# Kernel tuning notes

Measured on AMD Instinct MI355X. Metric: run time of the kernel, lower is better.

## Reference

```python
import jax, jax.numpy as jnp
import numpy as np

B, S, LC, DIM, H, FFN = 1, 3600, 512, 1536, 12, 8960
HD = DIM // H          # 128
GRID = (4, 30, 30)     # f*h*w == S
K_LEN = 9900           # hardcoded k_lens in SelfAttention.forward
EPS = 1e-6

def _rope_axis_angles(n_pos, dim):
    inv = 1.0 / np.power(10000.0, np.arange(0, dim, 2, dtype=np.float64) / dim)
    return np.outer(np.arange(n_pos), inv)

def _build_rope(grid, head_dim):
    c = head_dim // 2                      # 64
    c1, c2 = c - 2 * (c // 3), c // 3      # 22, 21 (Wan 3D rope split)
    f, h, w = grid
    af = _rope_axis_angles(f, 2 * c1)
    ah = _rope_axis_angles(h, 2 * c2)
    aw = _rope_axis_angles(w, 2 * c2)
    ang = np.concatenate([
        np.broadcast_to(af[:, None, None, :], (f, h, w, c1)),
        np.broadcast_to(ah[None, :, None, :], (f, h, w, c2)),
        np.broadcast_to(aw[None, None, :, :], (f, h, w, c2)),
    ], axis=-1).reshape(f * h * w, c)
    return np.cos(ang).astype(np.float32), np.sin(ang).astype(np.float32)

def setup_inputs():
    key = jax.random.key(0)
    ks = iter(jax.random.split(key, 40))
    cos, sin = _build_rope(GRID, HD)
    inp = {
        'x': jax.random.normal(next(ks), (B, S, DIM), dtype=jnp.float32),
        'context': jax.random.normal(next(ks), (B, LC, DIM), dtype=jnp.float32),
        't_mod': 0.1 * jax.random.normal(next(ks), (B, 6, DIM), dtype=jnp.float32),
        'rope_cos': jnp.asarray(cos), 'rope_sin': jnp.asarray(sin),
        'modulation': jax.random.normal(next(ks), (1, 6, DIM), dtype=jnp.float32) / DIM ** 0.5,
    }
    for p in ('sa', 'ca'):
        for w in ('q', 'k', 'v', 'o'):
            inp[p + '_' + w + 'w'] = 0.02 * jax.random.normal(next(ks), (DIM, DIM), dtype=jnp.float32)
            inp[p + '_' + w + 'b'] = jnp.zeros((DIM,), jnp.float32)
        inp[p + '_nq'] = jnp.ones((DIM,), jnp.float32)
        inp[p + '_nk'] = jnp.ones((DIM,), jnp.float32)
    inp['n3_w'] = jnp.ones((DIM,), jnp.float32)
    inp['n3_b'] = jnp.zeros((DIM,), jnp.float32)
    inp['ffn_w1'] = 0.02 * jax.random.normal(next(ks), (DIM, FFN), dtype=jnp.float32)
    inp['ffn_b1'] = jnp.zeros((FFN,), jnp.float32)
    inp['ffn_w2'] = 0.02 * jax.random.normal(next(ks), (FFN, DIM), dtype=jnp.float32)
    inp['ffn_b2'] = jnp.zeros((DIM,), jnp.float32)
    return inp

def _rms(x, w):
    x32 = x.astype(jnp.float32)
    n = x32 * jax.lax.rsqrt(jnp.mean(x32 * x32, axis=-1, keepdims=True) + EPS)
    return n.astype(x.dtype) * w

def _ln(x, w=None, b=None):
    mu = jnp.mean(x, axis=-1, keepdims=True)
    var = jnp.mean(jnp.square(x - mu), axis=-1, keepdims=True)
    y = (x - mu) * jax.lax.rsqrt(var + EPS)
    return y if w is None else y * w + b

def _rope(x, cos, sin):
    b, s, h, d = x.shape
    x2 = x.reshape(b, s, h, d // 2, 2)
    xe, xo = x2[..., 0], x2[..., 1]
    c, sn = cos[None, :, None, :], sin[None, :, None, :]
    return jnp.stack([xe * c - xo * sn, xe * sn + xo * c], axis=-1).reshape(b, s, h, d)

def _attn(q, k, v, k_len=None):
    # q,k,v: [B,S,H,D]
    scores = jnp.einsum('bqhd,bkhd->bhqk', q, k) * (q.shape[-1] ** -0.5)
    if k_len is not None:
        mask = jnp.arange(k.shape[1]) < k_len
        scores = jnp.where(mask[None, None, None, :], scores, jnp.finfo(scores.dtype).min)
    return jnp.einsum('bhqk,bkhd->bqhd', jax.nn.softmax(scores, axis=-1), v)

def reference(x, context, t_mod, rope_cos, rope_sin, modulation,
              sa_qw, sa_qb, sa_kw, sa_kb, sa_vw, sa_vb, sa_ow, sa_ob, sa_nq, sa_nk,
              ca_qw, ca_qb, ca_kw, ca_kb, ca_vw, ca_vb, ca_ow, ca_ob, ca_nq, ca_nk,
              n3_w, n3_b, ffn_w1, ffn_b1, ffn_w2, ffn_b2):
    mod = modulation + t_mod                      # [B,6,DIM]
    sh_msa, sc_msa, g_msa, sh_mlp, sc_mlp, g_mlp = [mod[:, i:i + 1] for i in range(6)]
    b = x.shape[0]
    # --- self-attention with AdaLN modulate + 3D RoPE + k_lens mask ---
    h = _ln(x) * (1 + sc_msa) + sh_msa
    q = _rms(h @ sa_qw + sa_qb, sa_nq).reshape(b, -1, H, HD)
    k = _rms(h @ sa_kw + sa_kb, sa_nk).reshape(b, -1, H, HD)
    v = (h @ sa_vw + sa_vb).reshape(b, -1, H, HD)
    a = _attn(_rope(q, rope_cos, rope_sin), _rope(k, rope_cos, rope_sin), v, k_len=K_LEN)
    x = x + g_msa * (a.reshape(b, -1, DIM) @ sa_ow + sa_ob)
    # --- cross-attention ---
    hc = _ln(x, n3_w, n3_b)
    q = _rms(hc @ ca_qw + ca_qb, ca_nq).reshape(b, -1, H, HD)
    k = _rms(context @ ca_kw + ca_kb, ca_nk).reshape(b, -1, H, HD)
    v = (context @ ca_vw + ca_vb).reshape(b, -1, H, HD)
    x = x + (_attn(q, k, v).reshape(b, -1, DIM) @ ca_ow + ca_ob)
    # --- gated FFN with AdaLN modulate ---
    h = _ln(x) * (1 + sc_mlp) + sh_mlp
    h = jax.nn.gelu(h @ ffn_w1 + ffn_b1, approximate=True) @ ffn_w2 + ffn_b2
    return x + g_mlp * h
```

## Files before the change

kernel.cpp:

```cpp
#include <hip/hip_runtime.h>
#include <cstdint>

#define S_LEN 3600
#define DMODEL 1536
#define LCTX 512
#define NH 12
#define HDIM 128
#define FFND 8960
#define SPAD_SELF 3648

typedef short v8s __attribute__((ext_vector_type(8)));
typedef float v4f __attribute__((ext_vector_type(4)));
typedef unsigned short u16b;
typedef unsigned int u32b;

#define AS1 __attribute__((address_space(1)))
#define AS3 __attribute__((address_space(3)))

__device__ __forceinline__ void gl_lds16(const void* g, void* l){
  __builtin_amdgcn_global_load_lds((AS1 const void*)g, (AS3 void*)l, 16, 0, 0);
}

__device__ __forceinline__ u16b f2b(float f){
  union { float f; u32b i; } x; x.f = f;
// ... 68 lines not shown
  int hd = tid >> 1, kc = (tid & 1) * 16;
  u16b* dst = Vt + ((size_t)h * HDIM + hd) * Spad + kb + kc;
  #pragma unroll
  for (int e = 0; e < 16; e += 2){
    u32b pk = ((u32b)t[kc + e][hd]) | (((u32b)t[kc + e + 1][hd]) << 16);
    *(u32b*)(dst + e) = pk;
  }
}

__global__ __launch_bounds__(256) void ln_mod(const float* __restrict__ X,
                                              const float* __restrict__ gamma,
                                              const float* __restrict__ beta,
                                              float gadd, u16b* __restrict__ out){
  int row = blockIdx.x;
  const float* xr = X + (size_t)row * DMODEL;
  int tid = threadIdx.x;
  float v[6]; float s1 = 0.f, s2 = 0.f;
  #pragma unroll
  for (int j = 0; j < 6; ++j){ v[j] = xr[tid + j * 256]; s1 += v[j]; s2 += v[j] * v[j]; }
  #pragma unroll
  for (int o = 1; o < 64; o <<= 1){ s1 += __shfl_xor(s1, o); s2 += __shfl_xor(s2, o); }
  __shared__ float red[8];
  int wid = tid >> 6, lane = tid & 63;
  if (!lane){ red[wid * 2] = s1; red[wid * 2 + 1] = s2; }
  __syncthreads();
  s1 = red[0] + red[2] + red[4] + red[6];
  s2 = red[1] + red[3] + red[5] + red[7];
  float mu = s1 / DMODEL;
  float var = s2 / DMODEL - mu * mu;
  float rstd = rsqrtf(var + 1e-6f);
  #pragma unroll
  for (int j = 0; j < 6; ++j){
    int c = tid + j * 256;
    float g = gamma[c] + gadd;
    float b = beta[c];
    out[(size_t)row * DMODEL + c] = f2b((v[j] - mu) * rstd * g + b);
  }
}

__global__ __launch_bounds__(256) void rms_rope(const float* __restrict__ X,
                                                const float* __restrict__ w,
                                                const float* __restrict__ cosT,
                                                const float* __restrict__ sinT,
                                                float qmul,
                                                u16b* __restrict__ out){
  int row = blockIdx.x;
  const float* xr = X + (size_t)row * DMODEL;
  int tid = threadIdx.x;
  float2 v[3]; float ss = 0.f;
  #pragma unroll
  for (int j = 0; j < 3; ++j){
    v[j] = *(const float2*)(xr + 2 * (tid + j * 256));
    ss += v[j].x * v[j].x + v[j].y * v[j].y;
  }
  #pragma unroll
  for (int o = 1; o < 64; o <<= 1) ss += __shfl_xor(ss, o);
  __shared__ float red[4];
  int wid = tid >> 6, lane = tid & 63;
  if (!lane) red[wid] = ss;
  __syncthreads();
  ss = red[0] + red[1] + red[2] + red[3];
  float rstd = rsqrtf(ss / DMODEL + 1e-6f);
  #pragma unroll
  for (int j = 0; j < 3; ++j){
    int p = tid + j * 256;
    float xe = v[j].x * rstd * w[2 * p];
    float xo = v[j].y * rstd * w[2 * p + 1];
    float oe, oo;
    if (cosT){
      int d = p & 63;
      float c = cosT[row * 64 + d], sn = sinT[row * 64 + d];
      oe = xe * c - xo * sn; oo = xe * sn + xo * c;
    } else { oe = xe; oo = xo; }
    oe *= qmul; oo *= qmul;
    u32b packed = ((u32b)f2b(oe)) | (((u32b)f2b(oo)) << 16);
    *(u32b*)(out + (size_t)row * DMODEL + 2 * p) = packed;
  }
}

struct Seg { const float* bias; float* outF; u16b* outB; };
struct Segs { Seg s[3]; };

template<int EPI>
__global__ __launch_bounds__(256, 2) void gemm_bt(
    const u16b* __restrict__ A, const u16b* __restrict__ BT,
    const float* __restrict__ bias, const float* __restrict__ res,
    const float* __restrict__ gate, float* __restrict__ outF,
    u16b* __restrict__ outB, int M, int N, int K, int kLen)
{
  __shared__ char Ls[3][16384];
  const int tid = threadIdx.x, lane = tid & 63, wid = tid >> 6;
  const int nwg = gridDim.x * gridDim.y;
  const int swz = xcd_swz(blockIdx.x + gridDim.x * blockIdx.y, nwg);
  const int bm = (swz % gridDim.x) * 128, bn = (swz / gridDim.x) * 128;
  const int kbase = blockIdx.z * kLen;
  const int wm = (wid >> 1) * 64, wn = (wid & 1) * 64;
  v4f acc[4][4] = {};

  auto stage = [&](int buf, int t){
    int k0 = kbase + t * 32;
    #pragma unroll
    for (int c = 0; c < 2; ++c){
      int seg = wid * 2 + c;
      int l = seg * 64 + lane;
      int row = l >> 2, cs = l & 3;
      int col = cs ^ swz4(row);
      gl_lds16(A + (size_t)min(bm + row, M - 1) * K + k0 + col * 8,
               Ls[buf] + seg * 1024);
      gl_lds16(BT + (size_t)(bn + row) * K + k0 + col * 8,
               Ls[buf] + 8192 + seg * 1024);
    }
  };

  const int nt = kLen / 32;
  stage(0, 0);
  stage(1, 1);
  const int chk = lane >> 4, qr = lane & 15;
  for (int t = 0; t < nt; ++t){
    if (t + 1 < nt) asm volatile("s_waitcnt vmcnt(4)" ::: "memory");
    else            asm volatile("s_waitcnt vmcnt(0)" ::: "memory");
    __builtin_amdgcn_s_barrier();
    if (t + 2 < nt) stage((t + 2) % 3, t + 2);
    char* Ab = Ls[t % 3]; char* Bb = Ab + 8192;
    v8s af[4], bfr[4];
    #pragma unroll
    for (int f = 0; f < 4; ++f){
      int rowa = wm + f * 16 + qr;
      af[f] = *(const v8s*)(Ab + rowa * 64 + ((chk ^ swz4(rowa)) * 16));
      int rowb = wn + f * 16 + qr;
      bfr[f] = *(const v8s*)(Bb + rowb * 64 + ((chk ^ swz4(rowb)) * 16));
    }
    __builtin_amdgcn_s_setprio(1);
    #pragma unroll
    for (int i = 0; i < 4; ++i)
      #pragma unroll
      for (int j = 0; j < 4; ++j)
        acc[i][j] = __builtin_amdgcn_mfma_f32_16x16x32_bf16(af[i], bfr[j], acc[i][j], 0, 0, 0);
    __builtin_amdgcn_s_setprio(0);
  }
  const int rr = lane >> 4;
  #pragma unroll
  for (int i = 0; i < 4; ++i){
    #pragma unroll
    for (int j = 0; j < 4; ++j){
      int n = bn + wn + j * 16 + qr;
      float bv = (EPI != 5 && bias) ? bias[n] : 0.f;
      float gv = (EPI == 2 && gate) ? gate[n] : 1.f;
      #pragma unroll
      for (int r = 0; r < 4; ++r){
        int m = bm + wm + i * 16 + rr * 4 + r;
        if (m < M){
          float val = acc[i][j][r] + bv;
          size_t idx = (size_t)m * N + n;
          if (EPI == 1) outF[idx] = val;
          else if (EPI == 2) outF[idx] = res[idx] + gv * val;
          else if (EPI == 5) outF[(size_t)blockIdx.z * M * N + idx] = val;
          else {
            float t3 = val * val * val;
            float g = val / (1.f + __expf(-1.5957691216057308f * (val + 0.044715f * t3)));
            outB[idx] = f2b(g);
          }
        }
      }
    }
  }
}

__global__ __launch_bounds__(256, 2) void gemm_seg(
    const u16b* __restrict__ A, const u16b* __restrict__ BT,
    Segs segs, int M, int N, int K)
{
  __shared__ char Ls[3][16384];
  const int tid = threadIdx.x, lane = tid & 63, wid = tid >> 6;
  const int nwg = gridDim.x * gridDim.y;
  const int swz = xcd_swz(blockIdx.x + gridDim.x * blockIdx.y, nwg);
  const int bm = (swz % gridDim.x) * 128, bn = (swz / gridDim.x) * 128;
  const int wm = (wid >> 1) * 64, wn = (wid & 1) * 64;
  v4f acc[4][4] = {};

  auto stage = [&](int buf, int t){
    int k0 = t * 32;
    #pragma unroll
    for (int c = 0; c < 2; ++c){
      int seg = wid * 2 + c;
      int l = seg * 64 + lane;
      int row = l >> 2, cs = l & 3;
      int col = cs ^ swz4(row);
      gl_lds16(A + (size_t)min(bm + row, M - 1) * K + k0 + col * 8,
               Ls[buf] + seg * 1024);
      gl_lds16(BT + (size_t)(bn + row) * K + k0 + col * 8,
               Ls[buf] + 8192 + seg * 1024);
    }
  };

  const int nt = K / 32;
  stage(0, 0);
  stage(1, 1);
  const int chk = lane >> 4, qr = lane & 15;
  for (int t = 0; t < nt; ++t){
    if (t + 1 < nt) asm volatile("s_waitcnt vmcnt(4)" ::: "memory");
    else            asm volatile("s_waitcnt vmcnt(0)" ::: "memory");
    __builtin_amdgcn_s_barrier();
    if (t + 2 < nt) stage((t + 2) % 3, t + 2);
    char* Ab = Ls[t % 3]; char* Bb = Ab + 8192;
    v8s af[4], bfr[4];
    #pragma unroll
    for (int f = 0; f < 4; ++f){
      int rowa = wm + f * 16 + qr;
      af[f] = *(const v8s*)(Ab + rowa * 64 + ((chk ^ swz4(rowa)) * 16));
      int rowb = wn + f * 16 + qr;
      bfr[f] = *(const v8s*)(Bb + rowb * 64 + ((chk ^ swz4(rowb)) * 16));
    }
    __builtin_amdgcn_s_setprio(1);
    #pragma unroll
    for (int i = 0; i < 4; ++i)
      #pragma unroll
      for (int j = 0; j < 4; ++j)
        acc[i][j] = __builtin_amdgcn_mfma_f32_16x16x32_bf16(af[i], bfr[j], acc[i][j], 0, 0, 0);
    __builtin_amdgcn_s_setprio(0);
  }
  const int seg = bn / 1536;
  const Seg sg = segs.s[seg];
  const int rr = lane >> 4;
  #pragma unroll
  for (int i = 0; i < 4; ++i){
    #pragma unroll
    for (int j = 0; j < 4; ++j){
      int nloc = bn - seg * 1536 + wn + j * 16 + qr;
      float bv = sg.bias[nloc];
      #pragma unroll
      for (int r = 0; r < 4; ++r){
        int m = bm + wm + i * 16 + rr * 4 + r;
        if (m < M){
          float val = acc[i][j][r] + bv;
          size_t idx = (size_t)m * 1536 + nloc;
          if (sg.outB) sg.outB[idx] = f2b(val);
          else sg.outF[idx] = val;
        }
      }
    }
  }
}

__global__ __launch_bounds__(256) void ffn2_reduce(const float* __restrict__ part,
                                                   const float* __restrict__ res,
                                                   const float* __restrict__ bias,
                                                   const float* __restrict__ gate,
                                                   float* __restrict__ out, int total){
  int i4 = blockIdx.x * 256 + threadIdx.x;
  if (i4 * 4 >= total) return;
  int base = i4 * 4;
  int n = base % DMODEL;
  float4 p0 = *(const float4*)(part + base);
  float4 p1 = *(const float4*)(part + (size_t)total + base);
  float4 p2 = *(const float4*)(part + 2 * (size_t)total + base);
  float4 p3 = *(const float4*)(part + 3 * (size_t)total + base);
  float4 rs = *(const float4*)(res + base);
  float4 bv = *(const float4*)(bias + n);
  float4 gv = *(const float4*)(gate + n);
  float4 o;
  o.x = rs.x + gv.x * (p0.x + p1.x + p2.x + p3.x + bv.x);
  o.y = rs.y + gv.y * (p0.y + p1.y + p2.y + p3.y + bv.y);
  o.z = rs.z + gv.z * (p0.z + p1.z + p2.z + p3.z + bv.z);
  o.w = rs.w + gv.w * (p0.w + p1.w + p2.w + p3.w + bv.w);
  *(float4*)(out + base) = o;
}

__global__ __launch_bounds__(256) void merge_o(const float* __restrict__ op0,
                                               const float* __restrict__ op1,
                                               const float2* __restrict__ ml,
                                               u16b* __restrict__ outO, int Sq){
  int i4 = blockIdx.x * 256 + threadIdx.x;
  const int perRow = DMODEL / 4;
  if (i4 >= Sq * perRow) return;
  int row = i4 / perRow, c4 = (i4 % perRow) * 4;
  int h = c4 >> 7;
  float2 ml0 = ml[h * Sq + row];
  float2 ml1 = ml[NH * Sq + h * Sq + row];
  float M = fmaxf(ml0.x, ml1.x);
  float w0 = exp2f(ml0.x - M), w1 = exp2f(ml1.x - M);
  float inv = 1.f / (ml0.y * w0 + ml1.y * w1);
  float4 a = *(const float4*)(op0 + (size_t)row * DMODEL + c4);
  float4 b = *(const float4*)(op1 + (size_t)row * DMODEL + c4);
  u32b lo = ((u32b)f2b((a.x * w0 + b.x * w1) * inv)) | (((u32b)f2b((a.y * w0 + b.y * w1) * inv)) << 16);
  u32b hi = ((u32b)f2b((a.z * w0 + b.z * w1) * inv)) | (((u32b)f2b((a.w * w0 + b.w * w1) * inv)) << 16);
  uint2 w2; w2.x = lo; w2.y = hi;
  *(uint2*)(outO + (size_t)row * DMODEL + c4) = w2;
}

__global__ __launch_bounds__(256, 4) void flash_attn(
    const u16b* __restrict__ Q, const u16b* __restrict__ Kp,
    const u16b* __restrict__ Vt, u16b* __restrict__ O,
    float* __restrict__ op0, float* __restrict__ op1,
    float2* __restrict__ mlbuf,
    int Sq, int Sk, int ksplit, int Spad)
{
  __shared__ char KV[32768];
  __shared__ char Pall[8192];
  const int tid = threadIdx.x, lane = tid & 63, wid = tid >> 6;
  const int h = blockIdx.y;
  const int z = blockIdx.z;
  const int kbeg = z * ksplit;
  const int kend = min(kbeg + ksplit, Sk);
  const int q0 = blockIdx.x * 64 + wid * 16;
  const int qq = lane & 15, cc = lane >> 4;
  char* Kb = KV; char* Vb = KV + 16384;
  char* Pb = Pall + wid * 2048;

  v8s qf[4];
  {
    int qrow = min(q0 + qq, Sq - 1);
    const u16b* qp = Q + (size_t)qrow * DMODEL + h * HDIM + cc * 8;
    #pragma unroll
    for (int ks = 0; ks < 4; ++ks) qf[ks] = *(const v8s*)(qp + ks * 32);
  }

  auto stage = [&](int kb0){
    #pragma unroll
    for (int c = 0; c < 4; ++c){
      int seg = wid * 4 + c;
      int g = seg * 64 + lane;
      int krow = g >> 4, kcol = (g & 15) ^ (krow & 7);
      gl_lds16(Kp + (size_t)min(kb0 + krow, Sk - 1) * DMODEL + h * HDIM + kcol * 8,
               Kb + seg * 1024);
// ... 116 lines not shown
        if (qrow < Sq)
          O[(size_t)qrow * DMODEL + h * HDIM + hdb * 16 + qq] = f2b(oacc[hdb][r] * lr[r]);
      }
  }
}

extern "C" void kernel_launch(void* const* d_in, const int* in_sizes, int n_in,
                              void* d_out, int out_size, void* d_ws, size_t ws_size,
                              hipStream_t stream){
  (void)in_sizes; (void)n_in; (void)out_size; (void)ws_size;
  const float* x     = (const float*)d_in[0];
  const float* ctx   = (const float*)d_in[1];
  const float* t_mod = (const float*)d_in[2];
  const float* ropec = (const float*)d_in[3];
  const float* ropes = (const float*)d_in[4];
  const float* modu  = (const float*)d_in[5];
  const float* sa_qw = (const float*)d_in[6];  const float* sa_qb = (const float*)d_in[7];
  const float* sa_kw = (const float*)d_in[8];  const float* sa_kb = (const float*)d_in[9];
  const float* sa_vw = (const float*)d_in[10]; const float* sa_vb = (const float*)d_in[11];
  const float* sa_ow = (const float*)d_in[12]; const float* sa_ob = (const float*)d_in[13];
  const float* sa_nq = (const float*)d_in[14]; const float* sa_nk = (const float*)d_in[15];
  const float* ca_qw = (const float*)d_in[16]; const float* ca_qb = (const float*)d_in[17];
  const float* ca_kw = (const float*)d_in[18]; const float* ca_kb = (const float*)d_in[19];
  const float* ca_vw = (const float*)d_in[20]; const float* ca_vb = (const float*)d_in[21];
  const float* ca_ow = (const float*)d_in[22]; const float* ca_ob = (const float*)d_in[23];
  const float* ca_nq = (const float*)d_in[24]; const float* ca_nk = (const float*)d_in[25];
  const float* n3w   = (const float*)d_in[26]; const float* n3b   = (const float*)d_in[27];
  const float* fw1   = (const float*)d_in[28]; const float* fb1   = (const float*)d_in[29];
  const float* fw2   = (const float*)d_in[30]; const float* fb2   = (const float*)d_in[31];
  float* out = (float*)d_out;

  const float QSCALE = 0.08838834764831845f * 1.4426950408889634f;

  char* wsp = (char*)d_ws;
  size_t off = 0;
  auto alloc = [&](size_t b){ void* p = wsp + off; off += (b + 255) & ~(size_t)255; return p; };
  const size_t WW = (size_t)DMODEL * DMODEL * 2;
  float* modc = (float*)alloc(6 * DMODEL * 4);
  u16b* w1T   = (u16b*)alloc((size_t)FFND * DMODEL * 2);
  u16b* w2T   = (u16b*)alloc((size_t)DMODEL * FFND * 2);
  u16b* h_bf  = (u16b*)alloc((size_t)S_LEN * DMODEL * 2);
  float* pre0 = (float*)alloc((size_t)S_LEN * DMODEL * 4);
  size_t region0 = off;
  u16b* sa_qkvT = (u16b*)alloc(3 * WW);
  u16b* sa_owT  = (u16b*)alloc(WW);
  u16b* ca_qwT  = (u16b*)alloc(WW);
  u16b* ca_kvT  = (u16b*)alloc(2 * WW);
  u16b* ca_owT  = (u16b*)alloc(WW);
  float* x2    = (float*)alloc((size_t)S_LEN * DMODEL * 4);
  float* pre2  = (float*)alloc((size_t)LCTX * DMODEL * 4);
  u16b* qb     = (u16b*)alloc((size_t)S_LEN * DMODEL * 2);
  u16b* kb     = (u16b*)alloc((size_t)S_LEN * DMODEL * 2);
  u16b* vb     = (u16b*)alloc((size_t)S_LEN * DMODEL * 2);
  u16b* ab     = (u16b*)alloc((size_t)S_LEN * DMODEL * 2);
  u16b* ctxb   = (u16b*)alloc((size_t)LCTX * DMODEL * 2);
  u16b* k2b    = (u16b*)alloc((size_t)LCTX * DMODEL * 2);
  u16b* v2b    = (u16b*)alloc((size_t)LCTX * DMODEL * 2);
  u16b* vts    = (u16b*)alloc((size_t)NH * HDIM * SPAD_SELF * 2);
  u16b* vtc    = (u16b*)alloc((size_t)NH * HDIM * LCTX * 2);
  u16b* fmid = (u16b*)(wsp + region0);
  float* fpart = (float*)(wsp + region0 + (size_t)S_LEN * FFND * 2);

  add_vec<<<36, 256, 0, stream>>>(modu, t_mod, modc, 6 * DMODEL);

  WJobs jobs; int t = 0;
  auto addjob = [&](int i, const float* w_, u16b* wt, int K, int N){
    jobs.j[i].W = w_; jobs.j[i].WT = wt; jobs.j[i].K = K; jobs.j[i].N = N; jobs.j[i].t0 = t;
    t += (K / 32) * (N / 32);
  };
  addjob(0, sa_qw, sa_qkvT, DMODEL, DMODEL);
  addjob(1, sa_kw, sa_qkvT + (size_t)DMODEL * DMODEL, DMODEL, DMODEL);
  addjob(2, sa_vw, sa_qkvT + (size_t)2 * DMODEL * DMODEL, DMODEL, DMODEL);
  addjob(3, sa_ow, sa_owT, DMODEL, DMODEL);
  addjob(4, ca_qw, ca_qwT, DMODEL, DMODEL);
  addjob(5, ca_kw, ca_kvT, DMODEL, DMODEL);
  addjob(6, ca_vw, ca_kvT + (size_t)DMODEL * DMODEL, DMODEL, DMODEL);
  addjob(7, ca_ow, ca_owT, DMODEL, DMODEL);
  addjob(8, fw1, w1T, DMODEL, FFND);
  addjob(9, fw2, w2T, FFND, DMODEL);
  wconv<<<t, 256, 0, stream>>>(jobs);

  f2b_kernel<<<(LCTX * DMODEL) / 256, 256, 0, stream>>>(ctx, ctxb, LCTX * DMODEL);

  ln_mod<<<S_LEN, 256, 0, stream>>>(x, modc + DMODEL, modc, 1.f, h_bf);
  dim3 g12(29, 12);
  {
    Segs sg;
    sg.s[0] = { sa_qb, pre0, nullptr };
    sg.s[1] = { sa_kb, x2,   nullptr };
    sg.s[2] = { sa_vb, nullptr, vb   };
    gemm_seg<<<dim3(29, 36), 256, 0, stream>>>(h_bf, sa_qkvT, sg, S_LEN, 3 * DMODEL, DMODEL);
  }
  rms_rope<<<S_LEN, 256, 0, stream>>>(pre0, sa_nq, ropec, ropes, QSCALE, qb);
  rms_rope<<<S_LEN, 256, 0, stream>>>(x2, sa_nk, ropec, ropes, 1.f, kb);
  vtrans<<<dim3(SPAD_SELF / 32, 12), 256, 0, stream>>>(vb, vts, S_LEN, SPAD_SELF);
  flash_attn<<<dim3(57, 12, 2), 256, 0, stream>>>(qb, kb, vts, ab,
      (float*)pre0, (float*)x2, (float2*)vb, S_LEN, S_LEN, 1856, SPAD_SELF);
  merge_o<<<(S_LEN * (DMODEL / 4) + 255) / 256, 256, 0, stream>>>(
      (const float*)pre0, (const float*)x2, (const float2*)vb, ab, S_LEN);
  gemm_bt<2><<<g12, 256, 0, stream>>>(ab, sa_owT, sa_ob, x, modc + 2 * DMODEL, x2, nullptr, S_LEN, DMODEL, DMODEL, DMODEL);

  ln_mod<<<S_LEN, 256, 0, stream>>>(x2, n3w, n3b, 0.f, h_bf);
  gemm_bt<1><<<g12, 256, 0, stream>>>(h_bf, ca_qwT, ca_qb, nullptr, nullptr, pre0, nullptr, S_LEN, DMODEL, DMODEL, DMODEL);
  {
    Segs sg;
    sg.s[0] = { ca_kb, pre2, nullptr };
    sg.s[1] = { ca_vb, nullptr, v2b  };
    sg.s[2] = { ca_vb, nullptr, v2b  };
    gemm_seg<<<dim3(4, 24), 256, 0, stream>>>(ctxb, ca_kvT, sg, LCTX, 2 * DMODEL, DMODEL);
  }
  rms_rope<<<S_LEN, 256, 0, stream>>>(pre0, ca_nq, nullptr, nullptr, QSCALE, qb);
  rms_rope<<<LCTX, 256, 0, stream>>>(pre2, ca_nk, nullptr, nullptr, 1.f, k2b);
  vtrans<<<dim3(16, 12), 256, 0, stream>>>(v2b, vtc, LCTX, LCTX);
  flash_attn<<<dim3(57, 12, 2), 256, 0, stream>>>(qb, k2b, vtc, ab,
      (float*)pre0, (float*)kb, (float2*)vts, S_LEN, LCTX, 256, LCTX);
  merge_o<<<(S_LEN * (DMODEL / 4) + 255) / 256, 256, 0, stream>>>(
      (const float*)pre0, (const float*)kb, (const float2*)vts, ab, S_LEN);
  gemm_bt<2><<<g12, 256, 0, stream>>>(ab, ca_owT, ca_ob, x2, nullptr, pre0, nullptr, S_LEN, DMODEL, DMODEL, DMODEL);

  ln_mod<<<S_LEN, 256, 0, stream>>>(pre0, modc + 4 * DMODEL, modc + 3 * DMODEL, 1.f, h_bf);
  gemm_bt<3><<<dim3(29, 70), 256, 0, stream>>>(h_bf, w1T, fb1, nullptr, nullptr, nullptr, fmid, S_LEN, FFND, DMODEL, DMODEL);
  gemm_bt<5><<<dim3(29, 12, 4), 256, 0, stream>>>(fmid, w2T, nullptr, nullptr, nullptr, fpart, nullptr, S_LEN, DMODEL, FFND, FFND / 4);
  ffn2_reduce<<<(S_LEN * DMODEL / 4 + 255) / 256, 256, 0, stream>>>(fpart, pre0, fb2, modc + 5 * DMODEL, out, S_LEN * DMODEL);
}
```

Baseline: 964.5 us.

## Add 128x256-tile GEMM for QKV and FFN, precompute load pointers and offsets

Adds a gemm_w kernel with 128x256 output tiles (each wave computes 64x128) and a 1D XCD-swizzled grid. It is used for the fused QKV projection, FFN up-projection with GELU, and the split-K FFN down-projection. The wider tile raises arithmetic intensity and reuse of the A tile in LDS, at the cost of more accumulator registers (32 v4f per wave) and 72KB of LDS per block, which may limit occupancy. The existing GEMMs also switch to precomputed, incrementing global pointers and precomputed LDS fragment offsets to cut address arithmetic in the inner loop.

```diff
diff --git a/kernel.cpp b/kernel.cpp
--- a/kernel.cpp
+++ b/kernel.cpp
@@ -174,6 +174,124 @@
 struct Segs { Seg s[3]; };
 
 template<int EPI>
+__global__ __launch_bounds__(256, 2) void gemm_w(
+    const u16b* __restrict__ A, const u16b* __restrict__ BT,
+    Segs segs, const float* __restrict__ bias,
+    float* __restrict__ outF, u16b* __restrict__ outB,
+    int M, int N, int K, int kLen, int nxM)
+{
+  __shared__ char Lsf[3 * 24576];
+  const int tid = threadIdx.x, lane = tid & 63, wid = tid >> 6;
+  const int swz = xcd_swz(blockIdx.x, gridDim.x);
+  const int bx = swz % nxM;
+  const int byz = swz / nxM;
+  const int nyN = N / 256;
+  const int by = (EPI == 2) ? (byz % nyN) : byz;
+  const int z  = (EPI == 2) ? (byz / nyN) : 0;
+  const int bm = bx * 128, bn = by * 256;
+  const int kbase = z * kLen;
+  const int wm = (wid >> 1) * 64, wn = (wid & 1) * 128;
+  const int qr = lane & 15, chk = lane >> 4;
+  v4f acc[4][8] = {};
+
+  const u16b* pA[2]; const u16b* pB[4];
+  #pragma unroll
+  for (int c = 0; c < 2; ++c){
+    int row = c * 64 + (tid >> 2);
+    int col = (tid & 3) ^ swz4(row);
+    pA[c] = A + (size_t)min(bm + row, M - 1) * K + kbase + col * 8;
+  }
+  #pragma unroll
+  for (int c = 0; c < 4; ++c){
+    int row = c * 64 + (tid >> 2);
+    int col = (tid & 3) ^ swz4(row);
+    pB[c] = BT + (size_t)(bn + row) * K + kbase + col * 8;
+  }
+  auto stage = [&](int b){
+    char* Lb = Lsf + b * 24576;
+    #pragma unroll
+    for (int c = 0; c < 2; ++c){
+      gl_lds16(pA[c], Lb + (c * 256 + tid) * 16);
+      pA[c] += 32;
+    }
+    #pragma unroll
+    for (int c = 0; c < 4; ++c){
+      gl_lds16(pB[c], Lb + 8192 + (c * 256 + tid) * 16);
+      pB[c] += 32;
+    }
+  };
+
+  int offA[4], offB[8];
+  #pragma unroll
+  for (int fr = 0; fr < 4; ++fr){
+    int r = wm + fr * 16 + qr;
+    offA[fr] = r * 64 + ((chk ^ swz4(r)) * 16);
+  }
+  #pragma unroll
+  for (int fc = 0; fc < 8; ++fc){
+    int r = wn + fc * 16 + qr;
+    offB[fc] = 8192 + r * 64 + ((chk ^ swz4(r)) * 16);
+  }
+
+  const int nt = kLen / 32;
+  stage(0); stage(1);
+  int s = 0, sp = 2;
+  for (int t = 0; t < nt; ++t){
+    if (t + 1 < nt) asm volatile("s_waitcnt vmcnt(6)" ::: "memory");
+    else            asm volatile("s_waitcnt vmcnt(0)" ::: "memory");
+    __builtin_amdgcn_s_barrier();
+    if (t + 2 < nt) stage(sp);
+    char* Lb = Lsf + s * 24576;
+    v8s af[4], bf[8];
+    #pragma unroll
+    for (int fr = 0; fr < 4; ++fr) af[fr] = *(const v8s*)(Lb + offA[fr]);
+    #pragma unroll
+    for (int fc = 0; fc < 8; ++fc) bf[fc] = *(const v8s*)(Lb + offB[fc]);
+    __builtin_amdgcn_s_setprio(1);
+    #pragma unroll
+    for (int fr = 0; fr < 4; ++fr)
+      #pragma unroll
+      for (int fc = 0; fc < 8; ++fc)
+        acc[fr][fc] = __builtin_amdgcn_mfma_f32_16x16x32_bf16(af[fr], bf[fc], acc[fr][fc], 0, 0, 0);
+    __builtin_amdgcn_s_setprio(0);
+    s = (s == 2) ? 0 : s + 1;
+    sp = (sp == 2) ? 0 : sp + 1;
+  }
+
+  const int rr = lane >> 4;
+  #pragma unroll
+  for (int fr = 0; fr < 4; ++fr){
+    #pragma unroll
+    for (int fc = 0; fc < 8; ++fc){
+      int n = bn + wn + fc * 16 + qr;
+      #pragma unroll
+      for (int r = 0; r < 4; ++r){
+        int m = bm + wm + fr * 16 + rr * 4 + r;
+        if (m < M){
+          float val = acc[fr][fc][r];
+          if (EPI == 0){
+            int sgi = n / 1536;
+            Seg sg = segs.s[sgi];
+            int nloc = n - sgi * 1536;
+            float v2 = val + sg.bias[nloc];
+            size_t idx = (size_t)m * 1536 + nloc;
+            if (sg.outB) sg.outB[idx] = f2b(v2);
+            else sg.outF[idx] = v2;
+          } else if (EPI == 1){
+            float v2 = val + bias[n];
+            float t3 = v2 * v2 * v2;
+            float g = v2 / (1.f + __expf(-1.5957691216057308f * (v2 + 0.044715f * t3)));
+            outB[(size_t)m * N + n] = f2b(g);
+          } else {
+            outF[(size_t)z * M * 1536 + (size_t)m * 1536 + n] = val;
+          }
+        }
+      }
+    }
+  }
+}
+
+template<int EPI>
 __global__ __launch_bounds__(256, 2) void gemm_bt(
     const u16b* __restrict__ A, const u16b* __restrict__ BT,
     const float* __restrict__ bias, const float* __restrict__ res,
@@ -189,38 +307,48 @@
   const int wm = (wid >> 1) * 64, wn = (wid & 1) * 64;
   v4f acc[4][4] = {};
 
-  auto stage = [&](int buf, int t){
-    int k0 = kbase + t * 32;
+  const u16b* pA[2]; const u16b* pB[2];
+  #pragma unroll
+  for (int c = 0; c < 2; ++c){
+    int row = c * 64 + (tid >> 2);
+    int col = (tid & 3) ^ swz4(row);
+    pA[c] = A + (size_t)min(bm + row, M - 1) * K + kbase + col * 8;
+    pB[c] = BT + (size_t)(bn + row) * K + kbase + col * 8;
+  }
+  auto stage = [&](int b){
+    char* Lb = Ls[b];
     #pragma unroll
     for (int c = 0; c < 2; ++c){
-      int seg = wid * 2 + c;
-      int l = seg * 64 + lane;
-      int row = l >> 2, cs = l & 3;
-      int col = cs ^ swz4(row);
-      gl_lds16(A + (size_t)min(bm + row, M - 1) * K + k0 + col * 8,
-               Ls[buf] + seg * 1024);
-      gl_lds16(BT + (size_t)(bn + row) * K + k0 + col * 8,
-               Ls[buf] + 8192 + seg * 1024);
+      gl_lds16(pA[c], Lb + (c * 256 + tid) * 16);
+      gl_lds16(pB[c], Lb + 8192 + (c * 256 + tid) * 16);
+      pA[c] += 32; pB[c] += 32;
     }
   };
 
+  const int chk = lane >> 4, qr = lane & 15;
+  int offA[4], offB[4];
+  #pragma unroll
+  for (int f = 0; f < 4; ++f){
+    int ra = wm + f * 16 + qr;
+    offA[f] = ra * 64 + ((chk ^ swz4(ra)) * 16);
+    int rb = wn + f * 16 + qr;
+    offB[f] = 8192 + rb * 64 + ((chk ^ swz4(rb)) * 16);
+  }
+
   const int nt = kLen / 32;
-  stage(0, 0);
-  stage(1, 1);
-  const int chk = lane >> 4, qr = lane & 15;
+  stage(0); stage(1);
+  int s = 0, sp = 2;
   for (int t = 0; t < nt; ++t){
     if (t + 1 < nt) asm volatile("s_waitcnt vmcnt(4)" ::: "memory");
     else            asm volatile("s_waitcnt vmcnt(0)" ::: "memory");
     __builtin_amdgcn_s_barrier();
-    if (t + 2 < nt) stage((t + 2) % 3, t + 2);
-    char* Ab = Ls[t % 3]; char* Bb = Ab + 8192;
+    if (t + 2 < nt) stage(sp);
+    char* Lb = Ls[s];
     v8s af[4], bfr[4];
     #pragma unroll
     for (int f = 0; f < 4; ++f){
-      int rowa = wm + f * 16 + qr;
-      af[f] = *(const v8s*)(Ab + rowa * 64 + ((chk ^ swz4(rowa)) * 16));
-      int rowb = wn + f * 16 + qr;
-      bfr[f] = *(const v8s*)(Bb + rowb * 64 + ((chk ^ swz4(rowb)) * 16));
+      af[f] = *(const v8s*)(Lb + offA[f]);
+      bfr[f] = *(const v8s*)(Lb + offB[f]);
     }
     __builtin_amdgcn_s_setprio(1);
     #pragma unroll
@@ -229,6 +357,8 @@
       for (int j = 0; j < 4; ++j)
         acc[i][j] = __builtin_amdgcn_mfma_f32_16x16x32_bf16(af[i], bfr[j], acc[i][j], 0, 0, 0);
     __builtin_amdgcn_s_setprio(0);
+    s = (s == 2) ? 0 : s + 1;
+    sp = (sp == 2) ? 0 : sp + 1;
   }
   const int rr = lane >> 4;
   #pragma unroll
@@ -236,7 +366,7 @@
     #pragma unroll
     for (int j = 0; j < 4; ++j){
       int n = bn + wn + j * 16 + qr;
-      float bv = (EPI != 5 && bias) ? bias[n] : 0.f;
+      float bv = bias ? bias[n] : 0.f;
       float gv = (EPI == 2 && gate) ? gate[n] : 1.f;
       #pragma unroll
       for (int r = 0; r < 4; ++r){
@@ -245,13 +375,7 @@
           float val = acc[i][j][r] + bv;
           size_t idx = (size_t)m * N + n;
           if (EPI == 1) outF[idx] = val;
-          else if (EPI == 2) outF[idx] = res[idx] + gv * val;
-          else if (EPI == 5) outF[(size_t)blockIdx.z * M * N + idx] = val;
-          else {
-            float t3 = val * val * val;
-            float g = val / (1.f + __expf(-1.5957691216057308f * (val + 0.044715f * t3)));
-            outB[idx] = f2b(g);
-          }
+          else outF[idx] = res[idx] + gv * val;
         }
       }
     }
@@ -270,38 +394,48 @@
   const int wm = (wid >> 1) * 64, wn = (wid & 1) * 64;
   v4f acc[4][4] = {};
 
-  auto stage = [&](int buf, int t){
-    int k0 = t * 32;
+  const u16b* pA[2]; const u16b* pB[2];
+  #pragma unroll
+  for (int c = 0; c < 2; ++c){
+    int row = c * 64 + (tid >> 2);
+    int col = (tid & 3) ^ swz4(row);
+    pA[c] = A + (size_t)min(bm + row, M - 1) * K + col * 8;
+    pB[c] = BT + (size_t)(bn + row) * K + col * 8;
+  }
+  auto stage = [&](int b){
+    char* Lb = Ls[b];
     #pragma unroll
     for (int c = 0; c < 2; ++c){
-      int seg = wid * 2 + c;
-      int l = seg * 64 + lane;
-      int row = l >> 2, cs = l & 3;
-      int col = cs ^ swz4(row);
-      gl_lds16(A + (size_t)min(bm + row, M - 1) * K + k0 + col * 8,
-               Ls[buf] + seg * 1024);
-      gl_lds16(BT + (size_t)(bn + row) * K + k0 + col * 8,
-               Ls[buf] + 8192 + seg * 1024);
+      gl_lds16(pA[c], Lb + (c * 256 + tid) * 16);
+      gl_lds16(pB[c], Lb + 8192 + (c * 256 + tid) * 16);
+      pA[c] += 32; pB[c] += 32;
     }
   };
 
+  const int chk = lane >> 4, qr = lane & 15;
+  int offA[4], offB[4];
+  #pragma unroll
+  for (int f = 0; f < 4; ++f){
+    int ra = wm + f * 16 + qr;
+    offA[f] = ra * 64 + ((chk ^ swz4(ra)) * 16);
+    int rb = wn + f * 16 + qr;
+    offB[f] = 8192 + rb * 64 + ((chk ^ swz4(rb)) * 16);
+  }
+
   const int nt = K / 32;
-  stage(0, 0);
-  stage(1, 1);
-  const int chk = lane >> 4, qr = lane & 15;
+  stage(0); stage(1);
+  int s = 0, sp = 2;
   for (int t = 0; t < nt; ++t){
     if (t + 1 < nt) asm volatile("s_waitcnt vmcnt(4)" ::: "memory");
     else            asm volatile("s_waitcnt vmcnt(0)" ::: "memory");
     __builtin_amdgcn_s_barrier();
-    if (t + 2 < nt) stage((t + 2) % 3, t + 2);
-    char* Ab = Ls[t % 3]; char* Bb = Ab + 8192;
+    if (t + 2 < nt) stage(sp);
+    char* Lb = Ls[s];
     v8s af[4], bfr[4];
     #pragma unroll
     for (int f = 0; f < 4; ++f){
-      int rowa = wm + f * 16 + qr;
-      af[f] = *(const v8s*)(Ab + rowa * 64 + ((chk ^ swz4(rowa)) * 16));
-      int rowb = wn + f * 16 + qr;
-      bfr[f] = *(const v8s*)(Bb + rowb * 64 + ((chk ^ swz4(rowb)) * 16));
+      af[f] = *(const v8s*)(Lb + offA[f]);
+      bfr[f] = *(const v8s*)(Lb + offB[f]);
     }
     __builtin_amdgcn_s_setprio(1);
     #pragma unroll
@@ -310,6 +444,8 @@
       for (int j = 0; j < 4; ++j)
         acc[i][j] = __builtin_amdgcn_mfma_f32_16x16x32_bf16(af[i], bfr[j], acc[i][j], 0, 0, 0);
     __builtin_amdgcn_s_setprio(0);
+    s = (s == 2) ? 0 : s + 1;
+    sp = (sp == 2) ? 0 : sp + 1;
   }
   const int seg = bn / 1536;
   const Seg sg = segs.s[seg];
@@ -614,6 +750,8 @@
 
   f2b_kernel<<<(LCTX * DMODEL) / 256, 256, 0, stream>>>(ctx, ctxb, LCTX * DMODEL);
 
+  Segs dummy = {};
+
   ln_mod<<<S_LEN, 256, 0, stream>>>(x, modc + DMODEL, modc, 1.f, h_bf);
   dim3 g12(29, 12);
   {
@@ -621,7 +759,8 @@
     sg.s[0] = { sa_qb, pre0, nullptr };
     sg.s[1] = { sa_kb, x2,   nullptr };
     sg.s[2] = { sa_vb, nullptr, vb   };
-    gemm_seg<<<dim3(29, 36), 256, 0, stream>>>(h_bf, sa_qkvT, sg, S_LEN, 3 * DMODEL, DMODEL);
+    gemm_w<0><<<29 * 18, 256, 0, stream>>>(h_bf, sa_qkvT, sg, nullptr, nullptr, nullptr,
+                                           S_LEN, 3 * DMODEL, DMODEL, DMODEL, 29);
   }
   rms_rope<<<S_LEN, 256, 0, stream>>>(pre0, sa_nq, ropec, ropes, QSCALE, qb);
   rms_rope<<<S_LEN, 256, 0, stream>>>(x2, sa_nk, ropec, ropes, 1.f, kb);
@@ -651,7 +790,9 @@
   gemm_bt<2><<<g12, 256, 0, stream>>>(ab, ca_owT, ca_ob, x2, nullptr, pre0, nullptr, S_LEN, DMODEL, DMODEL, DMODEL);
 
   ln_mod<<<S_LEN, 256, 0, stream>>>(pre0, modc + 4 * DMODEL, modc + 3 * DMODEL, 1.f, h_bf);
-  gemm_bt<3><<<dim3(29, 70), 256, 0, stream>>>(h_bf, w1T, fb1, nullptr, nullptr, nullptr, fmid, S_LEN, FFND, DMODEL, DMODEL);
-  gemm_bt<5><<<dim3(29, 12, 4), 256, 0, stream>>>(fmid, w2T, nullptr, nullptr, nullptr, fpart, nullptr, S_LEN, DMODEL, FFND, FFND / 4);
+  gemm_w<1><<<29 * 35, 256, 0, stream>>>(h_bf, w1T, dummy, fb1, nullptr, fmid,
+                                         S_LEN, FFND, DMODEL, DMODEL, 29);
+  gemm_w<2><<<29 * 6 * 4, 256, 0, stream>>>(fmid, w2T, dummy, nullptr, fpart, nullptr,
+                                            S_LEN, DMODEL, FFND, FFND / 4, 29);
   ffn2_reduce<<<(S_LEN * DMODEL / 4 + 255) / 256, 256, 0, stream>>>(fpart, pre0, fb2, modc + 5 * DMODEL, out, S_LEN * DMODEL);
 }
```

Result: slower. 1.036 ms (+7.4%).

## Split-K the 1536x1536 GEMMs into two halves and add a reduce kernel

Applied to the files above, without the earlier changes.

The three square DMODEL GEMMs (self-attn output, cross-attn Q, cross-attn output) now run split-K with two K-halves. This doubles the grid from 348 to 696 workgroups to fill more CUs. Each half writes fp32 partials into reused scratch buffers, and a new red2 kernel sums them and applies bias, gate and residual. The GEMM main loops also precompute global and LDS pointers/offsets instead of recomputing indices each iteration. The trade is extra partial-sum memory traffic and an added kernel launch per GEMM, plus reliance on aliasing scratch buffers (including the sa_qkvT weights buffer) that must be dead at that point.

```diff
diff --git a/kernel.cpp b/kernel.cpp
--- a/kernel.cpp
+++ b/kernel.cpp
@@ -176,9 +176,9 @@
 template<int EPI>
 __global__ __launch_bounds__(256, 2) void gemm_bt(
     const u16b* __restrict__ A, const u16b* __restrict__ BT,
-    const float* __restrict__ bias, const float* __restrict__ res,
-    const float* __restrict__ gate, float* __restrict__ outF,
-    u16b* __restrict__ outB, int M, int N, int K, int kLen)
+    const float* __restrict__ bias, float* __restrict__ outF,
+    float* __restrict__ outF2, u16b* __restrict__ outB,
+    int M, int N, int K, int kLen)
 {
   __shared__ char Ls[3][16384];
   const int tid = threadIdx.x, lane = tid & 63, wid = tid >> 6;
@@ -189,38 +189,48 @@
   const int wm = (wid >> 1) * 64, wn = (wid & 1) * 64;
   v4f acc[4][4] = {};
 
-  auto stage = [&](int buf, int t){
-    int k0 = kbase + t * 32;
+  const u16b* pA[2]; const u16b* pB[2];
+  #pragma unroll
+  for (int c = 0; c < 2; ++c){
+    int row = c * 64 + (tid >> 2);
+    int col = (tid & 3) ^ swz4(row);
+    pA[c] = A + (size_t)min(bm + row, M - 1) * K + kbase + col * 8;
+    pB[c] = BT + (size_t)(bn + row) * K + kbase + col * 8;
+  }
+  auto stage = [&](int b){
+    char* Lb = Ls[b];
     #pragma unroll
     for (int c = 0; c < 2; ++c){
-      int seg = wid * 2 + c;
-      int l = seg * 64 + lane;
-      int row = l >> 2, cs = l & 3;
-      int col = cs ^ swz4(row);
-      gl_lds16(A + (size_t)min(bm + row, M - 1) * K + k0 + col * 8,
-               Ls[buf] + seg * 1024);
-      gl_lds16(BT + (size_t)(bn + row) * K + k0 + col * 8,
-               Ls[buf] + 8192 + seg * 1024);
+      gl_lds16(pA[c], Lb + (c * 256 + tid) * 16);
+      gl_lds16(pB[c], Lb + 8192 + (c * 256 + tid) * 16);
+      pA[c] += 32; pB[c] += 32;
     }
   };
 
+  const int chk = lane >> 4, qr = lane & 15;
+  int offA[4], offB[4];
+  #pragma unroll
+  for (int f = 0; f < 4; ++f){
+    int ra = wm + f * 16 + qr;
+    offA[f] = ra * 64 + ((chk ^ swz4(ra)) * 16);
+    int rb = wn + f * 16 + qr;
+    offB[f] = 8192 + rb * 64 + ((chk ^ swz4(rb)) * 16);
+  }
+
   const int nt = kLen / 32;
-  stage(0, 0);
-  stage(1, 1);
-  const int chk = lane >> 4, qr = lane & 15;
+  stage(0); stage(1);
+  int s = 0, sp = 2;
   for (int t = 0; t < nt; ++t){
     if (t + 1 < nt) asm volatile("s_waitcnt vmcnt(4)" ::: "memory");
     else            asm volatile("s_waitcnt vmcnt(0)" ::: "memory");
     __builtin_amdgcn_s_barrier();
-    if (t + 2 < nt) stage((t + 2) % 3, t + 2);
-    char* Ab = Ls[t % 3]; char* Bb = Ab + 8192;
+    if (t + 2 < nt) stage(sp);
+    char* Lb = Ls[s];
     v8s af[4], bfr[4];
     #pragma unroll
     for (int f = 0; f < 4; ++f){
-      int rowa = wm + f * 16 + qr;
-      af[f] = *(const v8s*)(Ab + rowa * 64 + ((chk ^ swz4(rowa)) * 16));
-      int rowb = wn + f * 16 + qr;
-      bfr[f] = *(const v8s*)(Bb + rowb * 64 + ((chk ^ swz4(rowb)) * 16));
+      af[f] = *(const v8s*)(Lb + offA[f]);
+      bfr[f] = *(const v8s*)(Lb + offB[f]);
     }
     __builtin_amdgcn_s_setprio(1);
     #pragma unroll
@@ -229,28 +239,31 @@
       for (int j = 0; j < 4; ++j)
         acc[i][j] = __builtin_amdgcn_mfma_f32_16x16x32_bf16(af[i], bfr[j], acc[i][j], 0, 0, 0);
     __builtin_amdgcn_s_setprio(0);
+    s = (s == 2) ? 0 : s + 1;
+    sp = (sp == 2) ? 0 : sp + 1;
   }
   const int rr = lane >> 4;
+  float* op6 = (EPI == 6) ? (blockIdx.z ? outF2 : outF) : outF;
   #pragma unroll
   for (int i = 0; i < 4; ++i){
     #pragma unroll
     for (int j = 0; j < 4; ++j){
       int n = bn + wn + j * 16 + qr;
-      float bv = (EPI != 5 && bias) ? bias[n] : 0.f;
-      float gv = (EPI == 2 && gate) ? gate[n] : 1.f;
+      float bv = (EPI == 3) ? bias[n] : 0.f;
       #pragma unroll
       for (int r = 0; r < 4; ++r){
         int m = bm + wm + i * 16 + rr * 4 + r;
         if (m < M){
           float val = acc[i][j][r] + bv;
           size_t idx = (size_t)m * N + n;
-          if (EPI == 1) outF[idx] = val;
-          else if (EPI == 2) outF[idx] = res[idx] + gv * val;
-          else if (EPI == 5) outF[(size_t)blockIdx.z * M * N + idx] = val;
-          else {
+          if (EPI == 3){
             float t3 = val * val * val;
             float g = val / (1.f + __expf(-1.5957691216057308f * (val + 0.044715f * t3)));
             outB[idx] = f2b(g);
+          } else if (EPI == 5){
+            outF[(size_t)blockIdx.z * M * N + idx] = val;
+          } else {
+            op6[idx] = val;
           }
         }
       }
@@ -270,38 +283,48 @@
   const int wm = (wid >> 1) * 64, wn = (wid & 1) * 64;
   v4f acc[4][4] = {};
 
-  auto stage = [&](int buf, int t){
-    int k0 = t * 32;
+  const u16b* pA[2]; const u16b* pB[2];
+  #pragma unroll
+  for (int c = 0; c < 2; ++c){
+    int row = c * 64 + (tid >> 2);
+    int col = (tid & 3) ^ swz4(row);
+    pA[c] = A + (size_t)min(bm + row, M - 1) * K + col * 8;
+    pB[c] = BT + (size_t)(bn + row) * K + col * 8;
+  }
+  auto stage = [&](int b){
+    char* Lb = Ls[b];
     #pragma unroll
     for (int c = 0; c < 2; ++c){
-      int seg = wid * 2 + c;
-      int l = seg * 64 + lane;
-      int row = l >> 2, cs = l & 3;
-      int col = cs ^ swz4(row);
-      gl_lds16(A + (size_t)min(bm + row, M - 1) * K + k0 + col * 8,
-               Ls[buf] + seg * 1024);
-      gl_lds16(BT + (size_t)(bn + row) * K + k0 + col * 8,
-               Ls[buf] + 8192 + seg * 1024);
+      gl_lds16(pA[c], Lb + (c * 256 + tid) * 16);
+      gl_lds16(pB[c], Lb + 8192 + (c * 256 + tid) * 16);
+      pA[c] += 32; pB[c] += 32;
     }
   };
 
+  const int chk = lane >> 4, qr = lane & 15;
+  int offA[4], offB[4];
+  #pragma unroll
+  for (int f = 0; f < 4; ++f){
+    int ra = wm + f * 16 + qr;
+    offA[f] = ra * 64 + ((chk ^ swz4(ra)) * 16);
+    int rb = wn + f * 16 + qr;
+    offB[f] = 8192 + rb * 64 + ((chk ^ swz4(rb)) * 16);
+  }
+
   const int nt = K / 32;
-  stage(0, 0);
-  stage(1, 1);
-  const int chk = lane >> 4, qr = lane & 15;
+  stage(0); stage(1);
+  int s = 0, sp = 2;
   for (int t = 0; t < nt; ++t){
     if (t + 1 < nt) asm volatile("s_waitcnt vmcnt(4)" ::: "memory");
     else            asm volatile("s_waitcnt vmcnt(0)" ::: "memory");
     __builtin_amdgcn_s_barrier();
-    if (t + 2 < nt) stage((t + 2) % 3, t + 2);
-    char* Ab = Ls[t % 3]; char* Bb = Ab + 8192;
+    if (t + 2 < nt) stage(sp);
+    char* Lb = Ls[s];
     v8s af[4], bfr[4];
     #pragma unroll
     for (int f = 0; f < 4; ++f){
-      int rowa = wm + f * 16 + qr;
-      af[f] = *(const v8s*)(Ab + rowa * 64 + ((chk ^ swz4(rowa)) * 16));
-      int rowb = wn + f * 16 + qr;
-      bfr[f] = *(const v8s*)(Bb + rowb * 64 + ((chk ^ swz4(rowb)) * 16));
+      af[f] = *(const v8s*)(Lb + offA[f]);
+      bfr[f] = *(const v8s*)(Lb + offB[f]);
     }
     __builtin_amdgcn_s_setprio(1);
     #pragma unroll
@@ -310,6 +333,8 @@
       for (int j = 0; j < 4; ++j)
         acc[i][j] = __builtin_amdgcn_mfma_f32_16x16x32_bf16(af[i], bfr[j], acc[i][j], 0, 0, 0);
     __builtin_amdgcn_s_setprio(0);
+    s = (s == 2) ? 0 : s + 1;
+    sp = (sp == 2) ? 0 : sp + 1;
   }
   const int seg = bn / 1536;
   const Seg sg = segs.s[seg];
@@ -332,6 +357,30 @@
       }
     }
   }
+}
+
+__global__ __launch_bounds__(256) void red2(const float* __restrict__ p0,
+                                            const float* __restrict__ p1,
+                                            const float* __restrict__ res,
+                                            const float* __restrict__ gate,
+                                            const float* __restrict__ bias,
+                                            float* __restrict__ out, int total){
+  int i4 = blockIdx.x * 256 + threadIdx.x;
+  if (i4 * 4 >= total) return;
+  int base = i4 * 4, n = base % DMODEL;
+  float4 a = *(const float4*)(p0 + base);
+  float4 b = *(const float4*)(p1 + base);
+  float4 bv = *(const float4*)(bias + n);
+  float gx = 1.f, gy = 1.f, gz = 1.f, gw = 1.f;
+  if (gate){ float4 g = *(const float4*)(gate + n); gx = g.x; gy = g.y; gz = g.z; gw = g.w; }
+  float rx = 0.f, ry = 0.f, rz = 0.f, rw = 0.f;
+  if (res){ float4 r = *(const float4*)(res + base); rx = r.x; ry = r.y; rz = r.z; rw = r.w; }
+  float4 o;
+  o.x = rx + gx * (a.x + b.x + bv.x);
+  o.y = ry + gy * (a.y + b.y + bv.y);
+  o.z = rz + gz * (a.z + b.z + bv.z);
+  o.w = rw + gw * (a.w + b.w + bv.w);
+  *(float4*)(out + base) = o;
 }
 
 __global__ __launch_bounds__(256) void ffn2_reduce(const float* __restrict__ part,
@@ -614,8 +663,9 @@
 
   f2b_kernel<<<(LCTX * DMODEL) / 256, 256, 0, stream>>>(ctx, ctxb, LCTX * DMODEL);
 
+  const int RED_G = (S_LEN * DMODEL / 4 + 255) / 256;
+
   ln_mod<<<S_LEN, 256, 0, stream>>>(x, modc + DMODEL, modc, 1.f, h_bf);
-  dim3 g12(29, 12);
   {
     Segs sg;
     sg.s[0] = { sa_qb, pre0, nullptr };
@@ -628,12 +678,18 @@
   vtrans<<<dim3(SPAD_SELF / 32, 12), 256, 0, stream>>>(vb, vts, S_LEN, SPAD_SELF);
   flash_attn<<<dim3(57, 12, 2), 256, 0, stream>>>(qb, kb, vts, ab,
       (float*)pre0, (float*)x2, (float2*)vb, S_LEN, S_LEN, 1856, SPAD_SELF);
-  merge_o<<<(S_LEN * (DMODEL / 4) + 255) / 256, 256, 0, stream>>>(
+  merge_o<<<RED_G, 256, 0, stream>>>(
       (const float*)pre0, (const float*)x2, (const float2*)vb, ab, S_LEN);
-  gemm_bt<2><<<g12, 256, 0, stream>>>(ab, sa_owT, sa_ob, x, modc + 2 * DMODEL, x2, nullptr, S_LEN, DMODEL, DMODEL, DMODEL);
+  gemm_bt<6><<<dim3(29, 12, 2), 256, 0, stream>>>(ab, sa_owT, nullptr,
+      (float*)pre0, (float*)qb, nullptr, S_LEN, DMODEL, DMODEL, 768);
+  red2<<<RED_G, 256, 0, stream>>>((const float*)pre0, (const float*)qb,
+      x, modc + 2 * DMODEL, sa_ob, x2, S_LEN * DMODEL);
 
   ln_mod<<<S_LEN, 256, 0, stream>>>(x2, n3w, n3b, 0.f, h_bf);
-  gemm_bt<1><<<g12, 256, 0, stream>>>(h_bf, ca_qwT, ca_qb, nullptr, nullptr, pre0, nullptr, S_LEN, DMODEL, DMODEL, DMODEL);
+  gemm_bt<6><<<dim3(29, 12, 2), 256, 0, stream>>>(h_bf, ca_qwT, nullptr,
+      (float*)qb, (float*)vb, nullptr, S_LEN, DMODEL, DMODEL, 768);
+  red2<<<RED_G, 256, 0, stream>>>((const float*)qb, (const float*)vb,
+      nullptr, nullptr, ca_qb, pre0, S_LEN * DMODEL);
   {
     Segs sg;
     sg.s[0] = { ca_kb, pre2, nullptr };
@@ -646,12 +702,17 @@
   vtrans<<<dim3(16, 12), 256, 0, stream>>>(v2b, vtc, LCTX, LCTX);
   flash_attn<<<dim3(57, 12, 2), 256, 0, stream>>>(qb, k2b, vtc, ab,
       (float*)pre0, (float*)kb, (float2*)vts, S_LEN, LCTX, 256, LCTX);
-  merge_o<<<(S_LEN * (DMODEL / 4) + 255) / 256, 256, 0, stream>>>(
+  merge_o<<<RED_G, 256, 0, stream>>>(
       (const float*)pre0, (const float*)kb, (const float2*)vts, ab, S_LEN);
-  gemm_bt<2><<<g12, 256, 0, stream>>>(ab, ca_owT, ca_ob, x2, nullptr, pre0, nullptr, S_LEN, DMODEL, DMODEL, DMODEL);
+  gemm_bt<6><<<dim3(29, 12, 2), 256, 0, stream>>>(ab, ca_owT, nullptr,
+      (float*)qb, (float*)sa_qkvT, nullptr, S_LEN, DMODEL, DMODEL, 768);
+  red2<<<RED_G, 256, 0, stream>>>((const float*)qb, (const float*)sa_qkvT,
+      x2, nullptr, ca_ob, pre0, S_LEN * DMODEL);
 
   ln_mod<<<S_LEN, 256, 0, stream>>>(pre0, modc + 4 * DMODEL, modc + 3 * DMODEL, 1.f, h_bf);
-  gemm_bt<3><<<dim3(29, 70), 256, 0, stream>>>(h_bf, w1T, fb1, nullptr, nullptr, nullptr, fmid, S_LEN, FFND, DMODEL, DMODEL);
-  gemm_bt<5><<<dim3(29, 12, 4), 256, 0, stream>>>(fmid, w2T, nullptr, nullptr, nullptr, fpart, nullptr, S_LEN, DMODEL, FFND, FFND / 4);
-  ffn2_reduce<<<(S_LEN * DMODEL / 4 + 255) / 256, 256, 0, stream>>>(fpart, pre0, fb2, modc + 5 * DMODEL, out, S_LEN * DMODEL);
-}
+  gemm_bt<3><<<dim3(29, 70), 256, 0, stream>>>(h_bf, w1T, fb1,
+      nullptr, nullptr, fmid, S_LEN, FFND, DMODEL, DMODEL);
+  gemm_bt<5><<<dim3(29, 12, 4), 256, 0, stream>>>(fmid, w2T, nullptr,
+      fpart, nullptr, nullptr, S_LEN, DMODEL, FFND, FFND / 4);
+  ffn2_reduce<<<RED_G, 256, 0, stream>>>(fpart, pre0, fb2, modc + 5 * DMODEL, out, S_LEN * DMODEL);
+}
```

After: 949.2 us. No clear change (-1.6%).
